# Kernel optimization log

Hardware: AMD Instinct MI355X
Metric: run time of the kernel (lower is better)

## Reference

```python
import jax, jax.numpy as jnp
import numpy as np

B, S, D, BS = 256, 256, 448, 32
NB = D // BS  # 14 diagonal blocks


def setup_inputs() -> dict:
    key = jax.random.key(0)
    ks = jax.random.split(key, 9)
    xavier = float(np.sqrt(6.0 / (D + D)))
    inp = {
        "x": jax.random.normal(ks[0], (B, S, D), jnp.float32),
        "W_q": jax.random.uniform(ks[1], (D, D), jnp.float32, -xavier, xavier),
        "W_k": jax.random.uniform(ks[2], (D, D), jnp.float32, -xavier, xavier),
        "W_v": jax.random.uniform(ks[3], (D, D), jnp.float32, -xavier, xavier),
        "W_o": jax.random.uniform(ks[4], (D, D), jnp.float32, -xavier, xavier),
        "SSM_A": jnp.tril(jax.random.normal(ks[5], (D, D), jnp.float32) * 0.001),
        "SSM_B": jnp.tril(jax.random.normal(ks[6], (D, D), jnp.float32) * 0.001),
        "SSM_C": jnp.tril(jax.random.normal(ks[7], (D, D), jnp.float32) * 0.001),
        "dynamic_weight": jnp.full((1,), 0.5, jnp.float32),  # torch init value
        "ln_gamma": jnp.ones((D,), jnp.float32),
        "ln_beta": jnp.zeros((D,), jnp.float32),
    }
    return inp


def _diag_blocks(M):
    # extract the NB diagonal 32x32 blocks: [NB, BS, BS]
    idx = jnp.arange(NB)
    return M.reshape(NB, BS, NB, BS)[idx, :, idx, :]


def _block_linear(x, M):
    # block-diagonal matmul, vectorized over all 14 blocks at once
    xr = x.reshape(B, S, NB, BS)
    return jnp.einsum('bsni,nij->bsnj', xr, _diag_blocks(M)).reshape(B, S, D)


def _block_quadratic(x, M):
    # einsum('bsi,ij,bsk->bsj') per block == (x_blk @ M_blk) * sum_k(x_blk) * 0.1
    xr = x.reshape(B, S, NB, BS)
    y = jnp.einsum('bsni,nij->bsnj', xr, _diag_blocks(M))
    y = y * (jnp.sum(xr, axis=-1, keepdims=True) * 0.1)
    return y.reshape(B, S, D)


def _layer_norm(x, gamma, beta):
    mu = jnp.mean(x, axis=-1, keepdims=True)
    var = jnp.mean(jnp.square(x - mu), axis=-1, keepdims=True)
    return (x - mu) * jax.lax.rsqrt(var + 1e-5) * gamma + beta


def reference(x, W_q, W_k, W_v, W_o, SSM_A, SSM_B, SSM_C, dynamic_weight, ln_gamma, ln_beta):
    q = jnp.einsum('bsi,id->bsd', x, W_q)
    k = jnp.einsum('bsi,id->bsd', x, W_k)
    v = jnp.einsum('bsi,id->bsd', x, W_v)
    dw = jax.nn.sigmoid(dynamic_weight)  # sigmoid(0.5)=0.622 -> blended branch (seq_len == threshold)
    ssm_lin = _layer_norm(
        _block_linear(q, SSM_A) + _block_linear(k, SSM_B) + _block_linear(v, SSM_C),
        ln_gamma, ln_beta)
    ssm_quad = _layer_norm(
        _block_quadratic(q, SSM_A) + _block_quadratic(k, SSM_B) + _block_quadratic(v, SSM_C),
        ln_gamma, ln_beta)
    ssm = dw * ssm_quad + (1.0 - dw) * ssm_lin
    ssm = ssm + x  # residual; dropout is identity in eval mode
    return jnp.einsum('bsd,do->bso', ssm, W_o)
```

## Files before the change

kernel.cpp:

```cpp
#include <hip/hip_runtime.h>
#include <hip/hip_bf16.h>


typedef unsigned short u16;
typedef unsigned int u32;
typedef __bf16 bf16x8 __attribute__((ext_vector_type(8)));
typedef float f32x4 __attribute__((ext_vector_type(4)));

#define D_DIM 448
#define M_DIM 65536
#define NCAT 1386
#define NWCAT 1536
#define ZSTRIDE 1392
#define N2_PAD 512

#define CVT_BLKS 28672
#define WO_BLKS 896
#define WCAT_BLKS 1536

__device__ __forceinline__ u16 f2bf(float f) {
    union { float f; u32 u; } v; v.f = f;
    u32 u = v.u;
    return (u16)((u + 0x7fffu + ((u >> 16) & 1u)) >> 16);
}
__device__ __forceinline__ float bf2f(u16 h) {
    union { u32 u; float f; } v; v.u = ((u32)h) << 16;
    return v.f;
}
__device__ __forceinline__ void load_lds16(const void* g, void* l) {
    __builtin_amdgcn_global_load_lds(
        (const __attribute__((address_space(1))) void*)g,
        (__attribute__((address_space(3))) void*)l, 16, 0, 0);
}

__global__ __launch_bounds__(256) void prep_all(
    const float* __restrict__ x,
    const float* __restrict__ Wq, const float* __restrict__ Wk, const float* __restrict__ Wv,
    const float* __restrict__ Wo,
    const float* __restrict__ SA, const float* __restrict__ SB, const float* __restrict__ SC,
    u16* __restrict__ Xbf, u16* __restrict__ WcatT, u16* __restrict__ WoT)
{
    const int bid = blockIdx.x;
    const int tid = threadIdx.x;

    if (bid < CVT_BLKS) {
        const size_t i = ((size_t)bid * 256 + tid) * 4;
        float4 v = *reinterpret_cast<const float4*>(x + i);
        u32 lo = (u32)f2bf(v.x) | ((u32)f2bf(v.y) << 16);
        u32 hi = (u32)f2bf(v.z) | ((u32)f2bf(v.w) << 16);
        u32* p = reinterpret_cast<u32*>(Xbf + i);
        p[0] = lo; p[1] = hi;
        return;
    }
    if (bid < CVT_BLKS + WO_BLKS) {
        const int idx = (bid - CVT_BLKS) * 256 + tid;
        const int o = idx / D_DIM, d = idx % D_DIM;
        WoT[idx] = (o < D_DIM) ? f2bf(Wo[(size_t)d * D_DIM + o]) : (u16)0;
        return;
    }
    const int j = bid - (CVT_BLKS + WO_BLKS);
    u16* dst = WcatT + (size_t)j * D_DIM;
    if (j >= NCAT) {
        for (int t = tid; t < D_DIM; t += 256) dst[t] = 0;
        return;
    }
    if (j < 3 * D_DIM) {
        const int g = j / D_DIM, jj = j % D_DIM, n = jj >> 5;
        const float* W = (g == 0) ? Wq : (g == 1) ? Wk : Wv;
        const float* Mm = (g == 0) ? SA : (g == 1) ? SB : SC;
        __shared__ float av[32];
        if (tid < 32) av[tid] = Mm[(size_t)(n * 32 + tid) * D_DIM + jj];
        __syncthreads();
        for (int t = tid; t < D_DIM; t += 256) {
            const float* wrow = W + (size_t)t * D_DIM + n * 32;
            float s = 0.f;
            #pragma unroll
            for (int l = 0; l < 32; ++l) s += wrow[l] * av[l];
            dst[t] = f2bf(s);
        }
    } else {
        const int js = j - 3 * D_DIM;
        const int g = js / 14, n = js % 14;
        const float* W = (g == 0) ? Wq : (g == 1) ? Wk : Wv;
        for (int t = tid; t < D_DIM; t += 256) {
            const float* wrow = W + (size_t)t * D_DIM + n * 32;
            float s = 0.f;
            #pragma unroll
            for (int l = 0; l < 32; ++l) s += wrow[l];
            dst[t] = f2bf(0.1f * s);
        }
    }
}


#define VMW(N) do { asm volatile("s_waitcnt vmcnt(" #N ")" ::: "memory"); } while (0)

template<bool BF16OUT>
__global__ __launch_bounds__(512, 2) void gemm8p(
    const u16* __restrict__ A,
    const u16* __restrict__ Bt,
    void* __restrict__ Cout,
    int ldc, int ncstore, int ncolblk)
{
    extern __shared__ char ldsc[];
    const int tid = threadIdx.x;
    const int wave = tid >> 6, lane = tid & 63;
    const int lrow = lane & 15;
    const int wr = wave >> 2, wc = wave & 3;

    const int cpx = gridDim.x >> 3;
    const int bid = blockIdx.x;
    const int tt = (bid & 7) * cpx + (bid >> 3);
    const int bx = tt % ncolblk, by = tt / ncolblk;
    const int brow = by * 256, bcol = bx * 256;

    const int c0 = wave * 64 + lane;
    const int r0 = c0 >> 3, r1 = r0 + 64;
    const int sc0 = ((((c0 & 7) << 4) ^ ((r0 & 7) << 4)) >> 1);
    const int sc1 = ((((c0 & 7) << 4) ^ ((r1 & 7) << 4)) >> 1);
    const int off0 = r0 * D_DIM + sc0;
    const int off1 = r1 * D_DIM + sc1;

    u32 aoff[4][2], boff[2][2];
    #pragma unroll
    for (int mi = 0; mi < 4; ++mi) {
        const int r = wr * 64 + mi * 16 + lrow;
        #pragma unroll
        for (int ks = 0; ks < 2; ++ks) {
            const int cb = ks * 64 + ((lane >> 4) << 4);
            aoff[mi][ks] = (u32)(((r << 7) + cb) ^ ((r & 7) << 4));
        }
    }
    #pragma unroll
    for (int ni = 0; ni < 2; ++ni) {
        const int r = wc * 32 + ni * 16 + lrow;
        #pragma unroll
        for (int ks = 0; ks < 2; ++ks) {
            const int cb = ks * 64 + ((lane >> 4) << 4);
            boff[ni][ks] = (u32)(((r << 7) + cb) ^ ((r & 7) << 4));
        }
    }

    f32x4 acc[2][4][2][2];
    #pragma unroll
    for (int a0 = 0; a0 < 2; ++a0)
        #pragma unroll
        for (int a1 = 0; a1 < 4; ++a1)
            #pragma unroll
            for (int a2 = 0; a2 < 2; ++a2)
                #pragma unroll
                for (int a3 = 0; a3 < 2; ++a3) {
                    f32x4 z = {0.f, 0.f, 0.f, 0.f};
                    acc[a0][a1][a2][a3] = z;
                }

#define STAGE_HALF(PTR, G0, ISB, H, K0, NBUF) do { \
    const u16* _gs = (PTR) + (size_t)((G0) + (H) * 128) * D_DIM + (K0); \
    char* _lb = ldsc + (NBUF) * 65536 + (ISB) * 32768 + (H) * 16384 + wave * 1024; \
    load_lds16(_gs + off0, _lb); \
    load_lds16(_gs + off1, _lb + 8192); \
} while (0)

#define PHASE(BUF, MH, NH, VMEND, ...) do { \
    bf16x8 af[4][2], bfr[2][2]; \
    { \
        const char* _ab = ldsc + (BUF) * 65536 + (MH) * 16384; \
        _Pragma("unroll") \
        for (int mi = 0; mi < 4; ++mi) \
            _Pragma("unroll") \
            for (int ks = 0; ks < 2; ++ks) \
                af[mi][ks] = *reinterpret_cast<const bf16x8*>(_ab + aoff[mi][ks]); \
        const char* _bb = ldsc + (BUF) * 65536 + 32768 + (NH) * 16384; \
        _Pragma("unroll") \
        for (int ni = 0; ni < 2; ++ni) \
            _Pragma("unroll") \
            for (int ks = 0; ks < 2; ++ks) \
                bfr[ni][ks] = *reinterpret_cast<const bf16x8*>(_bb + boff[ni][ks]); \
    } \
    __VA_ARGS__; \
    __builtin_amdgcn_s_barrier(); \
    asm volatile("s_waitcnt lgkmcnt(0)" ::: "memory"); \
    __builtin_amdgcn_sched_barrier(0); \
    __builtin_amdgcn_s_setprio(1); \
    _Pragma("unroll") \
    for (int ni = 0; ni < 2; ++ni) \
        _Pragma("unroll") \
        for (int mi = 0; mi < 4; ++mi) \
            _Pragma("unroll") \
            for (int ks = 0; ks < 2; ++ks) \
                acc[MH][mi][NH][ni] = __builtin_amdgcn_mfma_f32_16x16x32_bf16( \
                    af[mi][ks], bfr[ni][ks], acc[MH][mi][NH][ni], 0, 0, 0); \
    __builtin_amdgcn_s_setprio(0); \
    VMEND; \
    __builtin_amdgcn_s_barrier(); \
} while (0)

    STAGE_HALF(A,  brow, 0, 0, 0, 0);
    STAGE_HALF(Bt, bcol, 1, 0, 0, 0);
    STAGE_HALF(Bt, bcol, 1, 1, 0, 0);
    STAGE_HALF(A,  brow, 0, 1, 0, 0);
    VMW(4);
    __builtin_amdgcn_s_barrier();

    for (int t = 0; t < 6; ++t) {
        const int buf = t & 1, nbuf = buf ^ 1;
        const int k1 = (t + 1) * 64;
        PHASE(buf, 0, 0, VMW(4), STAGE_HALF(A,  brow, 0, 0, k1, nbuf));
        PHASE(buf, 0, 1, VMW(4), STAGE_HALF(Bt, bcol, 1, 0, k1, nbuf));
        PHASE(buf, 1, 1, (void)0, STAGE_HALF(Bt, bcol, 1, 1, k1, nbuf));
        PHASE(buf, 1, 0, VMW(4), STAGE_HALF(A,  brow, 0, 1, k1, nbuf));
    }
    PHASE(0, 0, 0, VMW(2), (void)0);
    PHASE(0, 0, 1, VMW(0), (void)0);
    PHASE(0, 1, 1, (void)0, (void)0);
    PHASE(0, 1, 0, (void)0, (void)0);

#undef PHASE
#undef STAGE_HALF

    #pragma unroll
    for (int mh = 0; mh < 2; ++mh)
        #pragma unroll
        for (int mi = 0; mi < 4; ++mi)
            #pragma unroll
            for (int nh = 0; nh < 2; ++nh)
                #pragma unroll
                for (int ni = 0; ni < 2; ++ni) {
                    const int col = bcol + nh * 128 + wc * 32 + ni * 16 + lrow;
                    const int rbase = brow + mh * 128 + wr * 64 + mi * 16 + ((lane >> 4) << 2);
                    #pragma unroll
                    for (int r = 0; r < 4; ++r) {
                        const float v = acc[mh][mi][nh][ni][r];
                        if (BF16OUT) {
                            if (col < ncstore)
                                ((u16*)Cout)[(size_t)(rbase + r) * ldc + col] = f2bf(v);
                        } else {
                            if (col < ncstore)
                                ((float*)Cout)[(size_t)(rbase + r) * ldc + col] = v;
                        }
                    }
                }
}

__global__ __launch_bounds__(256) void ssm_epilogue(
    const u16* __restrict__ Z, const u16* __restrict__ xb,
    const float* __restrict__ gamma, const float* __restrict__ beta,
    const float* __restrict__ dynw, u16* __restrict__ ssm)
{
    const int row = blockIdx.x * 4 + (threadIdx.x >> 6);
    const int lane = threadIdx.x & 63;
    const u16* zr = Z + (size_t)row * ZSTRIDE;
    const float dwv = 1.0f / (1.0f + __expf(-dynw[0]));
    const bool act = lane < 56;
    const int j0 = lane * 8;
    const int n = lane >> 2;

    float sv = (lane < 42) ? bf2f(zr[1344 + lane]) : 0.f;
    const float sA = __shfl(sv, n);
    const float sB = __shfl(sv, 14 + n);
    const float sC = __shfl(sv, 28 + n);

    float L[8], Q[8];
    float s0 = 0.f, s1 = 0.f, s2 = 0.f, s3 = 0.f;
    if (act) {
        uint4 va = *reinterpret_cast<const uint4*>(zr + j0);
        uint4 vb = *reinterpret_cast<const uint4*>(zr + 448 + j0);
        uint4 vc = *reinterpret_cast<const uint4*>(zr + 896 + j0);
        const u32* pa = reinterpret_cast<const u32*>(&va);
        const u32* pb = reinterpret_cast<const u32*>(&vb);
        const u32* pc = reinterpret_cast<const u32*>(&vc);
        #pragma unroll
        for (int w = 0; w < 4; ++w) {
            #pragma unroll
            for (int h = 0; h < 2; ++h) {
                const int i = w * 2 + h;
                const float a = bf2f((u16)((pa[w] >> (16 * h)) & 0xffffu));
                const float b = bf2f((u16)((pb[w] >> (16 * h)) & 0xffffu));
                const float c = bf2f((u16)((pc[w] >> (16 * h)) & 0xffffu));
                const float Lv = a + b + c;
                const float Qv = a * sA + b * sB + c * sC;
                L[i] = Lv; Q[i] = Qv;
                s0 += Lv; s1 += Lv * Lv; s2 += Qv; s3 += Qv * Qv;
            }
        }
    } else {
        #pragma unroll
        for (int i = 0; i < 8; ++i) { L[i] = 0.f; Q[i] = 0.f; }
    }
    #pragma unroll
    for (int off = 32; off > 0; off >>= 1) {
        s0 += __shfl_xor(s0, off);
        s1 += __shfl_xor(s1, off);
        s2 += __shfl_xor(s2, off);
        s3 += __shfl_xor(s3, off);
    }
    const float inv = 1.0f / 448.0f;
    const float mu0 = s0 * inv, mu1 = s2 * inv;
    const float rs0 = rsqrtf(fmaxf(s1 * inv - mu0 * mu0, 0.f) + 1e-5f);
    const float rs1 = rsqrtf(fmaxf(s3 * inv - mu1 * mu1, 0.f) + 1e-5f);

    if (act) {
        float4 g0 = *reinterpret_cast<const float4*>(gamma + j0);
        float4 g1 = *reinterpret_cast<const float4*>(gamma + j0 + 4);
        float4 b0 = *reinterpret_cast<const float4*>(beta + j0);
        float4 b1 = *reinterpret_cast<const float4*>(beta + j0 + 4);
        float gv[8] = {g0.x, g0.y, g0.z, g0.w, g1.x, g1.y, g1.z, g1.w};
        float bv[8] = {b0.x, b0.y, b0.z, b0.w, b1.x, b1.y, b1.z, b1.w};
        uint4 vx = *reinterpret_cast<const uint4*>(xb + (size_t)row * D_DIM + j0);
        const u32* px = reinterpret_cast<const u32*>(&vx);
        u32 outw[4];
        #pragma unroll
        for (int w = 0; w < 4; ++w) {
            u16 h0, h1;
            {
                const int i = w * 2;
                const float xr = bf2f((u16)(px[w] & 0xffffu));
                const float ln = (L[i] - mu0) * rs0 * gv[i] + bv[i];
                const float qn = (Q[i] - mu1) * rs1 * gv[i] + bv[i];
                h0 = f2bf(dwv * qn + (1.0f - dwv) * ln + xr);
            }
            {
                const int i = w * 2 + 1;
                const float xr = bf2f((u16)(px[w] >> 16));
                const float ln = (L[i] - mu0) * rs0 * gv[i] + bv[i];
                const float qn = (Q[i] - mu1) * rs1 * gv[i] + bv[i];
                h1 = f2bf(dwv * qn + (1.0f - dwv) * ln + xr);
            }
            outw[w] = (u32)h0 | ((u32)h1 << 16);
        }
        uint4 ov = {outw[0], outw[1], outw[2], outw[3]};
        *reinterpret_cast<uint4*>(ssm + (size_t)row * D_DIM + j0) = ov;
    }
}

extern "C" void kernel_launch(void* const* d_in, const int* in_sizes, int n_in,
                              void* d_out, int out_size, void* d_ws, size_t ws_size,
                              hipStream_t stream) {
    const float* x    = (const float*)d_in[0];
    const float* Wq   = (const float*)d_in[1];
    const float* Wk   = (const float*)d_in[2];
    const float* Wv   = (const float*)d_in[3];
    const float* Wo   = (const float*)d_in[4];
    const float* SA   = (const float*)d_in[5];
    const float* SB   = (const float*)d_in[6];
    const float* SC   = (const float*)d_in[7];
    const float* dynw = (const float*)d_in[8];
    const float* gma  = (const float*)d_in[9];
    const float* bta  = (const float*)d_in[10];
    float* out = (float*)d_out;

    char* ws = (char*)d_ws;
    u16* Xbf   = (u16*)(ws);
    u16* WcatT = (u16*)(ws + 58720256);
    u16* WoT   = (u16*)(ws + 60096512);
    u16* Z     = (u16*)(ws + 60555264);

    (void)hipFuncSetAttribute(reinterpret_cast<const void*>(gemm8p<true>),
                              hipFuncAttributeMaxDynamicSharedMemorySize, 131072);
    (void)hipFuncSetAttribute(reinterpret_cast<const void*>(gemm8p<false>),
                              hipFuncAttributeMaxDynamicSharedMemorySize, 131072);

    prep_all<<<dim3(CVT_BLKS + WO_BLKS + WCAT_BLKS), dim3(256), 0, stream>>>(
        x, Wq, Wk, Wv, Wo, SA, SB, SC, Xbf, WcatT, WoT);

    gemm8p<true><<<dim3(1536), dim3(512), 131072, stream>>>(
        Xbf, WcatT, (void*)Z, ZSTRIDE, ZSTRIDE, 6);

    ssm_epilogue<<<dim3(M_DIM / 4), dim3(256), 0, stream>>>(Z, Xbf, gma, bta, dynw, Xbf);

    gemm8p<false><<<dim3(512), dim3(512), 131072, stream>>>(
        Xbf, WoT, (void*)out, 448, 448, 2);
}
```

Measured before the change: 429.8 us.

## Reuse LDS fragments across GEMM sub-phases and drop per-phase lgkm waits

Restructures the bf16 GEMM main loop so A fragments are loaded once per M-half and B fragments once per N-half, then reused across the four MFMA sub-phases instead of being reloaded every phase. This cuts LDS read traffic. It also removes the explicit lgkmcnt(0) wait and sched_barrier before each MFMA group, leaving the compiler to schedule LDS reads against MFMAs, with barriers kept as compiler memory fences. The cost is more live fragment registers, which could pressure occupancy under the 2-blocks launch bound, and a possible loss of explicit scheduling control.

Measured after the change: 452.5 us. 5.3% more time.

```diff
diff --git a/kernel.cpp b/kernel.cpp
--- a/kernel.cpp
+++ b/kernel.cpp
@@ -10,9 +10,7 @@
 #define D_DIM 448
 #define M_DIM 65536
 #define NCAT 1386
-#define NWCAT 1536
 #define ZSTRIDE 1392
-#define N2_PAD 512
 
 #define CVT_BLKS 28672
 #define WO_BLKS 896
@@ -94,6 +92,7 @@
 
 
 #define VMW(N) do { asm volatile("s_waitcnt vmcnt(" #N ")" ::: "memory"); } while (0)
+#define BAR do { asm volatile("" ::: "memory"); __builtin_amdgcn_s_barrier(); asm volatile("" ::: "memory"); } while (0)
 
 template<bool BF16OUT>
 __global__ __launch_bounds__(512, 2) void gemm8p(
@@ -154,6 +153,9 @@
                     acc[a0][a1][a2][a3] = z;
                 }
 
+    bf16x8 af[4][2];
+    bf16x8 bfr[2][2][2];
+
 #define STAGE_HALF(PTR, G0, ISB, H, K0, NBUF) do { \
     const u16* _gs = (PTR) + (size_t)((G0) + (H) * 128) * D_DIM + (K0); \
     char* _lb = ldsc + (NBUF) * 65536 + (ISB) * 32768 + (H) * 16384 + wave * 1024; \
@@ -161,26 +163,25 @@
     load_lds16(_gs + off1, _lb + 8192); \
 } while (0)
 
-#define PHASE(BUF, MH, NH, VMEND, ...) do { \
-    bf16x8 af[4][2], bfr[2][2]; \
-    { \
-        const char* _ab = ldsc + (BUF) * 65536 + (MH) * 16384; \
+#define LOAD_AF(BUF, MH) do { \
+    const char* _ab = ldsc + (BUF) * 65536 + (MH) * 16384; \
+    _Pragma("unroll") \
+    for (int mi = 0; mi < 4; ++mi) \
         _Pragma("unroll") \
-        for (int mi = 0; mi < 4; ++mi) \
-            _Pragma("unroll") \
-            for (int ks = 0; ks < 2; ++ks) \
-                af[mi][ks] = *reinterpret_cast<const bf16x8*>(_ab + aoff[mi][ks]); \
-        const char* _bb = ldsc + (BUF) * 65536 + 32768 + (NH) * 16384; \
+        for (int ks = 0; ks < 2; ++ks) \
+            af[mi][ks] = *reinterpret_cast<const bf16x8*>(_ab + aoff[mi][ks]); \
+} while (0)
+
+#define LOAD_B(BUF, NH) do { \
+    const char* _bb = ldsc + (BUF) * 65536 + 32768 + (NH) * 16384; \
+    _Pragma("unroll") \
+    for (int ni = 0; ni < 2; ++ni) \
         _Pragma("unroll") \
-        for (int ni = 0; ni < 2; ++ni) \
-            _Pragma("unroll") \
-            for (int ks = 0; ks < 2; ++ks) \
-                bfr[ni][ks] = *reinterpret_cast<const bf16x8*>(_bb + boff[ni][ks]); \
-    } \
-    __VA_ARGS__; \
-    __builtin_amdgcn_s_barrier(); \
-    asm volatile("s_waitcnt lgkmcnt(0)" ::: "memory"); \
-    __builtin_amdgcn_sched_barrier(0); \
+        for (int ks = 0; ks < 2; ++ks) \
+            bfr[NH][ni][ks] = *reinterpret_cast<const bf16x8*>(_bb + boff[ni][ks]); \
+} while (0)
+
+#define MFMA_PH(MH, NH) do { \
     __builtin_amdgcn_s_setprio(1); \
     _Pragma("unroll") \
     for (int ni = 0; ni < 2; ++ni) \
@@ -189,10 +190,22 @@
             _Pragma("unroll") \
             for (int ks = 0; ks < 2; ++ks) \
                 acc[MH][mi][NH][ni] = __builtin_amdgcn_mfma_f32_16x16x32_bf16( \
-                    af[mi][ks], bfr[ni][ks], acc[MH][mi][NH][ni], 0, 0, 0); \
+                    af[mi][ks], bfr[NH][ni][ks], acc[MH][mi][NH][ni], 0, 0, 0); \
     __builtin_amdgcn_s_setprio(0); \
-    VMEND; \
-    __builtin_amdgcn_s_barrier(); \
+} while (0)
+
+#define KTILE(BUF, K1, DOSTAGE, V1, V2, V4) do { \
+    LOAD_AF(BUF, 0); LOAD_B(BUF, 0); \
+    if (DOSTAGE) STAGE_HALF(A, brow, 0, 0, (K1), (BUF) ^ 1); \
+    MFMA_PH(0, 0); V1; BAR; \
+    LOAD_B(BUF, 1); \
+    if (DOSTAGE) STAGE_HALF(Bt, bcol, 1, 0, (K1), (BUF) ^ 1); \
+    MFMA_PH(0, 1); V2; BAR; \
+    LOAD_AF(BUF, 1); \
+    if (DOSTAGE) STAGE_HALF(Bt, bcol, 1, 1, (K1), (BUF) ^ 1); \
+    MFMA_PH(1, 1); BAR; \
+    if (DOSTAGE) STAGE_HALF(A, brow, 0, 1, (K1), (BUF) ^ 1); \
+    MFMA_PH(1, 0); V4; BAR; \
 } while (0)
 
     STAGE_HALF(A,  brow, 0, 0, 0, 0);
@@ -200,22 +213,19 @@
     STAGE_HALF(Bt, bcol, 1, 1, 0, 0);
     STAGE_HALF(A,  brow, 0, 1, 0, 0);
     VMW(4);
-    __builtin_amdgcn_s_barrier();
+    BAR;
 
     for (int t = 0; t < 6; ++t) {
-        const int buf = t & 1, nbuf = buf ^ 1;
+        const int buf = t & 1;
         const int k1 = (t + 1) * 64;
-        PHASE(buf, 0, 0, VMW(4), STAGE_HALF(A,  brow, 0, 0, k1, nbuf));
-        PHASE(buf, 0, 1, VMW(4), STAGE_HALF(Bt, bcol, 1, 0, k1, nbuf));
-        PHASE(buf, 1, 1, (void)0, STAGE_HALF(Bt, bcol, 1, 1, k1, nbuf));
-        PHASE(buf, 1, 0, VMW(4), STAGE_HALF(A,  brow, 0, 1, k1, nbuf));
-    }
-    PHASE(0, 0, 0, VMW(2), (void)0);
-    PHASE(0, 0, 1, VMW(0), (void)0);
-    PHASE(0, 1, 1, (void)0, (void)0);
-    PHASE(0, 1, 0, (void)0, (void)0);
-
-#undef PHASE
+        KTILE(buf, k1, 1, VMW(4), VMW(4), VMW(4));
+    }
+    KTILE(0, 0, 0, VMW(2), VMW(0), (void)0);
+
+#undef KTILE
+#undef MFMA_PH
+#undef LOAD_B
+#undef LOAD_AF
 #undef STAGE_HALF
 
     #pragma unroll
```
